# Performance work log

Measured on AMD Instinct MI355X. Metric: run time of the kernel, lower is better.

## Reference

```python
import jax, jax.numpy as jnp
import numpy as np

MODEL_SIZE = 1024
NUM_LAYERS = 8
HEADS = 16
MAX_LENGTH = 4096


def make_alibi_mask(heads, max_len):
    # grid[q,k] = k - q
    grid = (np.arange(max_len)[None, :] - np.arange(max_len)[:, None]).astype(np.float32)
    grid = np.broadcast_to(grid[None, :, :], (heads, max_len, max_len)).copy()
    head_mults = np.power(2.0, -np.linspace(0.0, 8.0, num=heads + 1)[1:]).astype(np.float32)
    grid *= head_mults[:, None, None]
    causal = np.tril(np.ones((max_len, max_len), dtype=np.float32))[None]
    grid = np.where(causal == 0, np.float32(-90000000.0), grid)
    return jnp.asarray(grid)


def layer_norm(x, gamma, beta, eps=1e-3):
    # keras LayerNormalization default epsilon=1e-3
    mu = jnp.mean(x, axis=-1, keepdims=True)
    var = jnp.var(x, axis=-1, keepdims=True)
    return (x - mu) * jax.lax.rsqrt(var + eps) * gamma + beta


def setup_inputs() -> dict:
    key = jax.random.key(0)
    ks = jax.random.split(key, 1 + NUM_LAYERS)
    B, S, D = 2, 2048, MODEL_SIZE
    x = jax.random.normal(ks[0], (B, S, D), dtype=jnp.float32)

    def dense(k, din, dout):
        k1, k2 = jax.random.split(k)
        lim = (6.0 / (din + dout)) ** 0.5
        W = jax.random.uniform(k1, (din, dout), jnp.float32, -lim, lim)
        b = jnp.zeros((dout,), jnp.float32)
        return W, b

    params = []
    for i in range(NUM_LAYERS):
        lk = jax.random.split(ks[1 + i], 5)
        wq, bq = dense(lk[0], D, D)
        wkv, bkv = dense(lk[1], D, 2 * D)
        wo, bo = dense(lk[2], D, D)
        w1, b1 = dense(lk[3], D, 4 * D)
        w2, b2 = dense(lk[4], 4 * D, D)
        ln_att = (jnp.ones((D,), jnp.float32), jnp.zeros((D,), jnp.float32))
        ln_ffn = (jnp.ones((D,), jnp.float32), jnp.zeros((D,), jnp.float32))
        params.append((wq, bq, wkv, bkv, wo, bo, w1, b1, w2, b2,
                       ln_att[0], ln_att[1], ln_ffn[0], ln_ffn[1]))
    final_ln = (jnp.ones((D,), jnp.float32), jnp.zeros((D,), jnp.float32))
    # flatten params into dict
    out = {"target_sequence": x, "final_gamma": final_ln[0], "final_beta": final_ln[1]}
    names = ["wq", "bq", "wkv", "bkv", "wo", "bo", "w1", "b1", "w2", "b2",
             "att_gamma", "att_beta", "ffn_gamma", "ffn_beta"]
    for j, n in enumerate(names):
        out[n] = jnp.stack([params[i][j] for i in range(NUM_LAYERS)])
    return out


def attention(x, wq, bq, wkv, bkv, wo, bo, mask):
    B, S, D = x.shape
    H = HEADS
    hd = D // H
    q = (x @ wq + bq).reshape(B, S, H, hd)
    kv = x @ wkv + bkv
    k, v = jnp.split(kv, 2, axis=-1)
    k = k.reshape(B, S, H, hd)
    v = v.reshape(B, S, H, hd)
    score = jnp.einsum("bqhd,bkhd->bhqk", q, k) * (1.0 / np.sqrt(hd))
    score = score + mask[None]
    attn = jax.nn.softmax(score, axis=-1)
    heads = jnp.einsum("bhqk,bkhd->bqhd", attn, v).reshape(B, S, D)
    return heads @ wo + bo


def reference(target_sequence, wq, bq, wkv, bkv, wo, bo, w1, b1, w2, b2,
              att_gamma, att_beta, ffn_gamma, ffn_beta, final_gamma, final_beta):
    S = target_sequence.shape[1]
    mask = make_alibi_mask(HEADS, MAX_LENGTH)[:, :S, :S]
    x = target_sequence
    for i in range(NUM_LAYERS):
        h = layer_norm(x, att_gamma[i], att_beta[i])
        x = x + attention(h, wq[i], bq[i], wkv[i], bkv[i], wo[i], bo[i], mask)
        h = layer_norm(x, ffn_gamma[i], ffn_beta[i])
        h = jax.nn.softplus(h @ w1[i] + b1[i]) @ w2[i] + b2[i]
        x = x + h
    return layer_norm(x, final_gamma, final_beta)
```

## Files before the change

### kernel.cpp

```cpp
#include <hip/hip_runtime.h>
#include <math.h>

#define DM 1024
#define SEQ 2048
#define BATCH 2
#define NHEAD 16
#define HDIM 64
#define NLAYER 8
#define FFDIM 4096
#define MROWS (BATCH*SEQ)
#define QSTR 3072

typedef __attribute__((ext_vector_type(8))) unsigned short short8;
typedef __attribute__((ext_vector_type(8))) __bf16 bf16x8;
typedef __attribute__((ext_vector_type(4))) float f32x4;

__device__ __forceinline__ float softplus_f(float x){
    const float t = __expf(-fabsf(x));
    return fmaxf(x, 0.0f) + __logf(1.0f + t);
}

__device__ __forceinline__ unsigned short f2bf(float f){
    unsigned u = __builtin_bit_cast(unsigned, f);
    u += 0x7fffu + ((u >> 16) & 1u);
    return (unsigned short)(u >> 16);
}

__device__ __forceinline__ void gload_lds16(const void* g, void* l){
    __builtin_amdgcn_global_load_lds(
        (const __attribute__((address_space(1))) unsigned int*)g,
        (__attribute__((address_space(3))) unsigned int*)l, 16, 0, 0);
}

__global__ __launch_bounds__(256) void tcast_kernel(
    const float* __restrict__ src, unsigned short* __restrict__ dst, int K, int N)
{
    __shared__ float tile[32][33];
    const int bn = blockIdx.x * 32, bk = blockIdx.y * 32;
    const int tx = threadIdx.x & 31, ty = threadIdx.x >> 5;
    #pragma unroll
    for (int i = 0; i < 32; i += 8)
        tile[ty + i][tx] = src[(size_t)(bk + ty + i) * N + bn + tx];
    __syncthreads();
    #pragma unroll
    for (int i = 0; i < 32; i += 8)
        dst[(size_t)(bn + ty + i) * K + bk + tx] = f2bf(tile[tx][ty + i]);
}

__global__ __launch_bounds__(256) void bias_concat_kernel(
    const float* __restrict__ bq, const float* __restrict__ bkv, float* __restrict__ dst)
{
    const int i = blockIdx.x * 256 + threadIdx.x;
    const int l = i / QSTR, c = i % QSTR;
    dst[i] = (c < DM) ? bq[l * DM + c] : bkv[l * 2 * DM + (c - DM)];
}

__global__ __launch_bounds__(256) void vtrans_kernel(
    const unsigned short* __restrict__ qkv, unsigned short* __restrict__ vt)
{
    __shared__ unsigned short tile[64][72];
    const int b  = blockIdx.z;
    const int c0 = blockIdx.x * 64;
    const int s0 = blockIdx.y * 64;
    const int r  = threadIdx.x >> 2;
    const int cq = (threadIdx.x & 3) * 16;
    {
        const unsigned short* src = qkv + (size_t)(b*SEQ + s0 + r) * QSTR + 2*DM + c0 + cq;
        *(uint4*)&tile[r][cq]     = *(const uint4*)(src);
        *(uint4*)&tile[r][cq + 8] = *(const uint4*)(src + 8);
    }
    __syncthreads();
    unsigned short tmp[16];
    #pragma unroll
    for (int j = 0; j < 16; j++) tmp[j] = tile[cq + j][r];
    unsigned short* dst = vt + (size_t)(b*DM + c0 + r) * SEQ + s0 + cq;
    *(uint4*)(dst)     = *(const uint4*)&tmp[0];
    *(uint4*)(dst + 8) = *(const uint4*)&tmp[8];
}

template<bool OUT_BF16>
__global__ __launch_bounds__(256) void ln_kernel(
    const float* __restrict__ x, const float* __restrict__ gamma,
    const float* __restrict__ beta, void* __restrict__ outv)
{
    const int row = blockIdx.x;
    const int t = threadIdx.x;
    const float4 v = ((const float4*)(x + (size_t)row * DM))[t];
    float s  = v.x + v.y + v.z + v.w;
    float s2 = v.x*v.x + v.y*v.y + v.z*v.z + v.w*v.w;
    #pragma unroll
    for (int off = 32; off > 0; off >>= 1){
        s  += __shfl_down(s,  off);
        s2 += __shfl_down(s2, off);
    }
    __shared__ float red[8];
    const int wid = t >> 6;
    if ((t & 63) == 0){ red[wid] = s; red[4 + wid] = s2; }
    __syncthreads();
    if (t == 0){
        red[0] = red[0] + red[1] + red[2] + red[3];
        red[4] = red[4] + red[5] + red[6] + red[7];
    }
    __syncthreads();
    const float mean = red[0] * (1.0f / DM);
    const float var  = red[4] * (1.0f / DM) - mean * mean;
    const float rstd = rsqrtf(var + 1e-3f);
    const float4 g  = ((const float4*)gamma)[t];
    const float4 bt = ((const float4*)beta)[t];
    float ox = (v.x - mean) * rstd * g.x + bt.x;
    float oy = (v.y - mean) * rstd * g.y + bt.y;
    float oz = (v.z - mean) * rstd * g.z + bt.z;
    float ow = (v.w - mean) * rstd * g.w + bt.w;
    if (OUT_BF16){
        ushort4 o = make_ushort4(f2bf(ox), f2bf(oy), f2bf(oz), f2bf(ow));
        *(ushort4*)((unsigned short*)outv + (size_t)row * DM + t*4) = o;
    } else {
        ((float4*)((float*)outv + (size_t)row * DM))[t] = make_float4(ox, oy, oz, ow);
    }
}

template<bool SOFTPLUS, bool RESIDUAL, bool OUT_BF16>
__global__ __launch_bounds__(256) void gemm_bf16_kernel(
    const unsigned short* __restrict__ A, const unsigned short* __restrict__ Bt,
    const float* __restrict__ bias, const float* __restrict__ resid,
    void* __restrict__ Cv, int N, int K)
{
    __shared__ __align__(16) unsigned short As[2][128 * 32];
    __shared__ __align__(16) unsigned short Bs[2][128 * 32];
    const int t = threadIdx.x;
    const int lane = t & 63, w = t >> 6;
    const int bm = blockIdx.y * 128, bn = blockIdx.x * 128;

    const int srow = lane >> 2;
    const int scol = (lane & 3) * 8;
    const unsigned short* a_g0 = A  + (size_t)(bm + w*32 + srow) * K + scol;
    const unsigned short* a_g1 = a_g0 + (size_t)16 * K;
    const unsigned short* b_g0 = Bt + (size_t)(bn + w*32 + srow) * K + scol;
    const unsigned short* b_g1 = b_g0 + (size_t)16 * K;
    const int a_off0 = (w*32     ) * 32;
    const int a_off1 = (w*32 + 16) * 32;

    const int wr = (w >> 1) * 64;
    const int wc = (w & 1) * 64;
    const int fm = lane & 15;
    const int fq = (lane >> 4) * 8;

    f32x4 acc[4][4] = {};

#define STAGE(buf, k0)                                     \
    do {                                                   \
        gload_lds16(a_g0 + (k0), &As[buf][a_off0]);        \
        gload_lds16(a_g1 + (k0), &As[buf][a_off1]);        \
        gload_lds16(b_g0 + (k0), &Bs[buf][a_off0]);        \
        gload_lds16(b_g1 + (k0), &Bs[buf][a_off1]);        \
    } while (0)

#define COMPUTE(buf)                                                        \
    do {                                                                    \
        bf16x8 af[4], bfr[4];                                               \
        _Pragma("unroll")                                                   \
        for (int mi = 0; mi < 4; mi++)                                      \
            af[mi] = __builtin_bit_cast(bf16x8,                             \
                *(const short8*)&As[buf][(wr + mi*16 + fm) * 32 + fq]);     \
        _Pragma("unroll")                                                   \
        for (int ni = 0; ni < 4; ni++)                                      \
            bfr[ni] = __builtin_bit_cast(bf16x8,                            \
                *(const short8*)&Bs[buf][(wc + ni*16 + fm) * 32 + fq]);     \
        _Pragma("unroll")                                                   \
        for (int mi = 0; mi < 4; mi++)                                      \
            _Pragma("unroll")                                               \
            for (int ni = 0; ni < 4; ni++)                                  \
                acc[mi][ni] = __builtin_amdgcn_mfma_f32_16x16x32_bf16(      \
                    af[mi], bfr[ni], acc[mi][ni], 0, 0, 0);                 \
    } while (0)

    STAGE(0, 0);
    __syncthreads();
    for (int k0 = 0; k0 < K; k0 += 64){
        STAGE(1, k0 + 32);
        COMPUTE(0);
        __syncthreads();
        if (k0 + 64 < K) STAGE(0, k0 + 64);
        COMPUTE(1);
        __syncthreads();
    }
#undef STAGE
#undef COMPUTE

    const int crow = (lane >> 4) * 4;
    const int ccol = lane & 15;
    #pragma unroll
    for (int mi = 0; mi < 4; mi++){
        #pragma unroll
        for (int r = 0; r < 4; r++){
            const size_t row = (size_t)bm + wr + mi*16 + crow + r;
            #pragma unroll
            for (int ni = 0; ni < 4; ni++){
                const int col = bn + wc + ni*16 + ccol;
                float v = acc[mi][ni][r] + bias[col];
                if (SOFTPLUS) v = softplus_f(v);
                if (RESIDUAL) v += resid[row * N + col];
                if (OUT_BF16) ((unsigned short*)Cv)[row * N + col] = f2bf(v);
                else          ((float*)Cv)[row * N + col] = v;
            }
        }
    }
}

__global__ __launch_bounds__(256, 4) void attn_kernel(
    const unsigned short* __restrict__ qkv,
    const unsigned short* __restrict__ vt,
    unsigned short* __restrict__ outg)
{
    __shared__ __align__(16) unsigned short Qs[64][72];
    __shared__ __align__(16) unsigned short Ks[64][72];
    __shared__ __align__(16) unsigned short Vt[64][72];
    __shared__ __align__(16) unsigned short Ps[64][72];

    const int L   = blockIdx.x + 32 * (blockIdx.y + 16 * blockIdx.z);
    const int rep = L >> 8, jj = L & 255;
    const int mm  = jj >> 4, h = jj & 15;
    const int b   = rep >> 1;
    const int qt  = (rep & 1) ? (31 - mm) : mm;

    const int t = threadIdx.x;
    const int lane = t & 63, w = t >> 6;
    const int g = lane >> 4, s = lane & 15;

    const size_t qrow0 = (size_t)(b * SEQ + qt * 64);
    const int srow = t >> 2, slc = t & 3;

    {
        const unsigned short* src = qkv + (qrow0 + srow) * QSTR + h*HDIM + slc*16;
        *(uint4*)&Qs[srow][slc*16]     = *(const uint4*)(src);
        *(uint4*)&Qs[srow][slc*16 + 8] = *(const uint4*)(src + 8);
    }
    __syncthreads();
    bf16x8 qf0 = __builtin_bit_cast(bf16x8, *(const short8*)&Qs[w*16 + s][g*8]);
    bf16x8 qf1 = __builtin_bit_cast(bf16x8, *(const short8*)&Qs[w*16 + s][32 + g*8]);

    const float LOG2E  = 1.4426950408889634f;
    const float qscale = 0.125f * LOG2E;
    const float slope  = exp2f(-0.5f * (float)(h + 1)) * LOG2E;
    const int qi = qt*64 + w*16 + s;
    float m_i = -1e30f, l_i = 0.0f;
    f32x4 accO[4] = {};

    const unsigned short* vbase = vt + (size_t)(b*DM + h*HDIM + srow) * SEQ;

    for (int kt = 0; kt <= qt; kt++){
        __syncthreads();
        {
            const unsigned short* src =
                qkv + (size_t)(b*SEQ + kt*64 + srow) * QSTR + DM + h*HDIM + slc*16;
            *(uint4*)&Ks[srow][slc*16]     = *(const uint4*)(src);
            *(uint4*)&Ks[srow][slc*16 + 8] = *(const uint4*)(src + 8);
        }
        {
            const unsigned short* src = vbase + kt*64 + slc*16;
            *(uint4*)&Vt[srow][slc*16]     = *(const uint4*)(src);
            *(uint4*)&Vt[srow][slc*16 + 8] = *(const uint4*)(src + 8);
        }
        __syncthreads();

        f32x4 sacc[4] = {};
        #pragma unroll
        for (int mi = 0; mi < 4; mi++){
            bf16x8 kf0 = __builtin_bit_cast(bf16x8, *(const short8*)&Ks[mi*16 + s][g*8]);
            bf16x8 kf1 = __builtin_bit_cast(bf16x8, *(const short8*)&Ks[mi*16 + s][32 + g*8]);
            sacc[mi] = __builtin_amdgcn_mfma_f32_16x16x32_bf16(kf0, qf0, sacc[mi], 0, 0, 0);
            sacc[mi] = __builtin_amdgcn_mfma_f32_16x16x32_bf16(kf1, qf1, sacc[mi], 0, 0, 0);
        }

        float sc[16];
        const float bb = slope * (float)(kt*64 - qi);
        #pragma unroll
        for (int mi = 0; mi < 4; mi++)
            #pragma unroll
            for (int r = 0; r < 4; r++)
                sc[mi*4 + r] = fmaf(sacc[mi][r], qscale,
                                    fmaf(slope, (float)(mi*16 + g*4 + r), bb));
        if (kt == qt){
            #pragma unroll
            for (int mi = 0; mi < 4; mi++)
                #pragma unroll
                for (int r = 0; r < 4; r++)
                    if (mi*16 + g*4 + r > w*16 + s) sc[mi*4 + r] = -1e30f;
        }
        float mloc = sc[0];
        #pragma unroll
        for (int e = 1; e < 16; e++) mloc = fmaxf(mloc, sc[e]);
        mloc = fmaxf(mloc, __shfl_xor(mloc, 16));
        mloc = fmaxf(mloc, __shfl_xor(mloc, 32));

        float nm;
        if (__all(mloc - m_i <= 8.0f)){
            nm = m_i;
        } else {
            nm = fmaxf(m_i, mloc);
            const float alpha = exp2f(m_i - nm);
            m_i = nm;
            float av[4];
            #pragma unroll
            for (int r = 0; r < 4; r++) av[r] = __shfl(alpha, g*4 + r);
            #pragma unroll
            for (int ni = 0; ni < 4; ni++)
                #pragma unroll
                for (int r = 0; r < 4; r++) accO[ni][r] *= av[r];
            l_i *= alpha;
        }

        float rsum = 0.0f;
        #pragma unroll
        for (int mi = 0; mi < 4; mi++){
            const float p0 = exp2f(sc[mi*4+0] - nm);
            const float p1 = exp2f(sc[mi*4+1] - nm);
            const float p2 = exp2f(sc[mi*4+2] - nm);
            const float p3 = exp2f(sc[mi*4+3] - nm);
            rsum += (p0 + p1) + (p2 + p3);
            *(ushort4*)&Ps[w*16 + s][mi*16 + g*4] =
                make_ushort4(f2bf(p0), f2bf(p1), f2bf(p2), f2bf(p3));
        }
        rsum += __shfl_xor(rsum, 16);
        rsum += __shfl_xor(rsum, 32);
        l_i += rsum;

        bf16x8 pf0 = __builtin_bit_cast(bf16x8, *(const short8*)&Ps[w*16 + s][g*8]);
        bf16x8 pf1 = __builtin_bit_cast(bf16x8, *(const short8*)&Ps[w*16 + s][32 + g*8]);
        #pragma unroll
        for (int ni = 0; ni < 4; ni++){
            bf16x8 vf0 = __builtin_bit_cast(bf16x8, *(const short8*)&Vt[ni*16 + s][g*8]);
            bf16x8 vf1 = __builtin_bit_cast(bf16x8, *(const short8*)&Vt[ni*16 + s][32 + g*8]);
            accO[ni] = __builtin_amdgcn_mfma_f32_16x16x32_bf16(pf0, vf0, accO[ni], 0, 0, 0);
            accO[ni] = __builtin_amdgcn_mfma_f32_16x16x32_bf16(pf1, vf1, accO[ni], 0, 0, 0);
        }
    }

    float lv[4];
    #pragma unroll
    for (int r = 0; r < 4; r++) lv[r] = 1.0f / __shfl(l_i, g*4 + r);
    #pragma unroll
    for (int ni = 0; ni < 4; ni++)
        #pragma unroll
        for (int r = 0; r < 4; r++)
            outg[(qrow0 + w*16 + g*4 + r) * DM + h*HDIM + ni*16 + s] =
                f2bf(accO[ni][r] * lv[r]);
}

extern "C" void kernel_launch(void* const* d_in, const int* in_sizes, int n_in,
                              void* d_out, int out_size, void* d_ws, size_t ws_size,
                              hipStream_t stream)
{
    (void)in_sizes; (void)n_in; (void)out_size; (void)ws_size;

    const float* x_in = (const float*)d_in[0];
    const float* fg   = (const float*)d_in[1];
    const float* fb   = (const float*)d_in[2];
    const float* wq   = (const float*)d_in[3];
    const float* bq   = (const float*)d_in[4];
    const float* wkv  = (const float*)d_in[5];
    const float* bkv  = (const float*)d_in[6];
    const float* wo   = (const float*)d_in[7];
    const float* bo   = (const float*)d_in[8];
    const float* w1   = (const float*)d_in[9];
    const float* b1   = (const float*)d_in[10];
    const float* w2   = (const float*)d_in[11];
    const float* b2   = (const float*)d_in[12];
    const float* attg = (const float*)d_in[13];
    const float* attb = (const float*)d_in[14];
    const float* ffng = (const float*)d_in[15];
    const float* ffnb = (const float*)d_in[16];

    float* x = (float*)d_out;

    char* wp = (char*)d_ws;
    unsigned short* qkvbuf = (unsigned short*)wp; wp += (size_t)MROWS*QSTR*2;
    unsigned short* h1buf  = (unsigned short*)wp; wp += (size_t)MROWS*FFDIM*2;
    unsigned short* hbuf   = (unsigned short*)wp; wp += (size_t)MROWS*DM*2;
    unsigned short* attbuf = (unsigned short*)wp; wp += (size_t)MROWS*DM*2;
    unsigned short* wt_qkv = (unsigned short*)wp; wp += (size_t)QSTR*DM*2;
    unsigned short* wt_o   = (unsigned short*)wp; wp += (size_t)DM*DM*2;
    unsigned short* wt_1   = (unsigned short*)wp; wp += (size_t)FFDIM*DM*2;
    unsigned short* wt_2   = (unsigned short*)wp; wp += (size_t)DM*FFDIM*2;
    float*          qkv_b  = (float*)wp;          wp += (size_t)NLAYER*QSTR*4;

    unsigned short* vtbuf = h1buf;

    hipMemcpyAsync(x, x_in, (size_t)MROWS*DM*sizeof(float),
                   hipMemcpyDeviceToDevice, stream);
    bias_concat_kernel<<<NLAYER*QSTR/256, 256, 0, stream>>>(bq, bkv, qkv_b);

    const dim3 blk(256);
    const dim3 g_qkv(QSTR/128,  MROWS/128);
    const dim3 g_sq (DM/128,    MROWS/128);
    const dim3 g_ff (FFDIM/128, MROWS/128);
    const dim3 g_at (SEQ/64, NHEAD, BATCH);
    const dim3 g_vt (DM/64, SEQ/64, BATCH);

    for (int i = 0; i < NLAYER; i++){
        const float* wq_i  = wq  + (size_t)i*DM*DM;
        const float* wkv_i = wkv + (size_t)i*DM*2*DM;
        const float* wo_i  = wo  + (size_t)i*DM*DM;
        const float* bo_i  = bo  + (size_t)i*DM;
        const float* w1_i  = w1  + (size_t)i*DM*FFDIM;
        const float* b1_i  = b1  + (size_t)i*FFDIM;
        const float* w2_i  = w2  + (size_t)i*FFDIM*DM;
        const float* b2_i  = b2  + (size_t)i*DM;

        tcast_kernel<<<dim3(DM/32,    DM/32),    blk, 0, stream>>>(wq_i,  wt_qkv,         DM,    DM);
        tcast_kernel<<<dim3(2*DM/32,  DM/32),    blk, 0, stream>>>(wkv_i, wt_qkv + DM*DM, DM,    2*DM);
        tcast_kernel<<<dim3(DM/32,    DM/32),    blk, 0, stream>>>(wo_i,  wt_o,           DM,    DM);
        tcast_kernel<<<dim3(FFDIM/32, DM/32),    blk, 0, stream>>>(w1_i,  wt_1,           DM,    FFDIM);
        tcast_kernel<<<dim3(DM/32,    FFDIM/32), blk, 0, stream>>>(w2_i,  wt_2,           FFDIM, DM);

        ln_kernel<true><<<MROWS, blk, 0, stream>>>(x, attg + (size_t)i*DM, attb + (size_t)i*DM, hbuf);
        gemm_bf16_kernel<false,false,true><<<g_qkv, blk, 0, stream>>>(
            hbuf, wt_qkv, qkv_b + (size_t)i*QSTR, nullptr, qkvbuf, QSTR, DM);
        vtrans_kernel<<<g_vt, blk, 0, stream>>>(qkvbuf, vtbuf);
        attn_kernel<<<g_at, blk, 0, stream>>>(qkvbuf, vtbuf, attbuf);
        gemm_bf16_kernel<false,true,false><<<g_sq, blk, 0, stream>>>(
            attbuf, wt_o, bo_i, x, x, DM, DM);
        ln_kernel<true><<<MROWS, blk, 0, stream>>>(x, ffng + (size_t)i*DM, ffnb + (size_t)i*DM, hbuf);
        gemm_bf16_kernel<true,false,true><<<g_ff, blk, 0, stream>>>(
            hbuf, wt_1, b1_i, nullptr, h1buf, FFDIM, DM);
        gemm_bf16_kernel<false,true,false><<<g_sq, blk, 0, stream>>>(
            h1buf, wt_2, b2_i, x, x, DM, FFDIM);
    }
    ln_kernel<false><<<MROWS, blk, 0, stream>>>(x, fg, fb, x);
}
```

Measured before the change: 2.803 ms.

## Restructure bf16 GEMM with BK=64 swizzled LDS, register-prefetch pipeline and block remap

The GEMM K-tile grows from 32 to 64 and the LDS layout gets an XOR swizzle to avoid bank conflicts on fragment reads. The main loop now loads all fragments into registers, then immediately reissues the next global-to-LDS stage into the same buffer so the loads overlap the MFMAs. It uses explicit vmcnt/lgkmcnt waits in place of full syncthreads. Block indices are remapped across groups of 8 for better L2 locality, and launch bounds request 2 blocks per CU. This doubles LDS use (64KB) and raises register pressure.

```diff
diff --git a/kernel.cpp b/kernel.cpp
--- a/kernel.cpp
+++ b/kernel.cpp
@@ -120,72 +120,93 @@
 }
 
 template<bool SOFTPLUS, bool RESIDUAL, bool OUT_BF16>
-__global__ __launch_bounds__(256) void gemm_bf16_kernel(
+__global__ __launch_bounds__(256, 2) void gemm_bf16_kernel(
     const unsigned short* __restrict__ A, const unsigned short* __restrict__ Bt,
     const float* __restrict__ bias, const float* __restrict__ resid,
     void* __restrict__ Cv, int N, int K)
 {
-    __shared__ __align__(16) unsigned short As[2][128 * 32];
-    __shared__ __align__(16) unsigned short Bs[2][128 * 32];
+    __shared__ __align__(16) unsigned short As[2][128 * 64];
+    __shared__ __align__(16) unsigned short Bs[2][128 * 64];
     const int t = threadIdx.x;
     const int lane = t & 63, w = t >> 6;
-    const int bm = blockIdx.y * 128, bn = blockIdx.x * 128;
-
-    const int srow = lane >> 2;
-    const int scol = (lane & 3) * 8;
-    const unsigned short* a_g0 = A  + (size_t)(bm + w*32 + srow) * K + scol;
-    const unsigned short* a_g1 = a_g0 + (size_t)16 * K;
-    const unsigned short* b_g0 = Bt + (size_t)(bn + w*32 + srow) * K + scol;
-    const unsigned short* b_g1 = b_g0 + (size_t)16 * K;
-    const int a_off0 = (w*32     ) * 32;
-    const int a_off1 = (w*32 + 16) * 32;
+
+    const int gx = gridDim.x;
+    const int nwg = gx * gridDim.y;
+    int bid = blockIdx.x + gx * blockIdx.y;
+    bid = (bid & 7) * (nwg >> 3) + (bid >> 3);
+    const int bm = (bid / gx) * 128, bn = (bid % gx) * 128;
+
+    const int srow  = w*8 + (lane >> 3);
+    const int sslot = (lane & 7) ^ (lane >> 3);
+    const unsigned short* a_g = A  + (size_t)(bm + srow) * K + sslot * 8;
+    const unsigned short* b_g = Bt + (size_t)(bn + srow) * K + sslot * 8;
 
     const int wr = (w >> 1) * 64;
     const int wc = (w & 1) * 64;
     const int fm = lane & 15;
-    const int fq = (lane >> 4) * 8;
+    const int q  = lane >> 4;
+    const int f7 = fm & 7;
 
     f32x4 acc[4][4] = {};
-
-#define STAGE(buf, k0)                                     \
-    do {                                                   \
-        gload_lds16(a_g0 + (k0), &As[buf][a_off0]);        \
-        gload_lds16(a_g1 + (k0), &As[buf][a_off1]);        \
-        gload_lds16(b_g0 + (k0), &Bs[buf][a_off0]);        \
-        gload_lds16(b_g1 + (k0), &Bs[buf][a_off1]);        \
+    const int ntile = K >> 6;
+
+#define STAGE(buf, k0)                                                      \
+    do {                                                                    \
+        _Pragma("unroll")                                                   \
+        for (int j = 0; j < 4; j++){                                        \
+            gload_lds16(a_g + (size_t)(j*32)*K + (k0), &As[buf][(j*32 + w*8)*64]); \
+            gload_lds16(b_g + (size_t)(j*32)*K + (k0), &Bs[buf][(j*32 + w*8)*64]); \
+        }                                                                   \
     } while (0)
 
-#define COMPUTE(buf)                                                        \
-    do {                                                                    \
-        bf16x8 af[4], bfr[4];                                               \
+#define LOADFRAGS(buf)                                                      \
+    _Pragma("unroll")                                                       \
+    for (int kk2 = 0; kk2 < 2; kk2++){                                      \
         _Pragma("unroll")                                                   \
         for (int mi = 0; mi < 4; mi++)                                      \
-            af[mi] = __builtin_bit_cast(bf16x8,                             \
-                *(const short8*)&As[buf][(wr + mi*16 + fm) * 32 + fq]);     \
+            af[kk2][mi] = __builtin_bit_cast(bf16x8, *(const short8*)       \
+                &As[buf][(wr + mi*16 + fm)*64 + (((kk2*4 + q) ^ f7) << 3)]);\
         _Pragma("unroll")                                                   \
         for (int ni = 0; ni < 4; ni++)                                      \
-            bfr[ni] = __builtin_bit_cast(bf16x8,                            \
-                *(const short8*)&Bs[buf][(wc + ni*16 + fm) * 32 + fq]);     \
+            bfm[kk2][ni] = __builtin_bit_cast(bf16x8, *(const short8*)      \
+                &Bs[buf][(wc + ni*16 + fm)*64 + (((kk2*4 + q) ^ f7) << 3)]);\
+    }
+
+#define MFMAS()                                                             \
+    _Pragma("unroll")                                                       \
+    for (int kk2 = 0; kk2 < 2; kk2++)                                       \
         _Pragma("unroll")                                                   \
         for (int mi = 0; mi < 4; mi++)                                      \
             _Pragma("unroll")                                               \
             for (int ni = 0; ni < 4; ni++)                                  \
                 acc[mi][ni] = __builtin_amdgcn_mfma_f32_16x16x32_bf16(      \
-                    af[mi], bfr[ni], acc[mi][ni], 0, 0, 0);                 \
-    } while (0)
+                    af[kk2][mi], bfm[kk2][ni], acc[mi][ni], 0, 0, 0);
 
     STAGE(0, 0);
-    __syncthreads();
-    for (int k0 = 0; k0 < K; k0 += 64){
-        STAGE(1, k0 + 32);
-        COMPUTE(0);
-        __syncthreads();
-        if (k0 + 64 < K) STAGE(0, k0 + 64);
-        COMPUTE(1);
-        __syncthreads();
+    STAGE(1, 64);
+
+    int cur = 0;
+    for (int td = 0; td < ntile - 1; ++td){
+        asm volatile("s_waitcnt vmcnt(8)" ::: "memory");
+        __builtin_amdgcn_s_barrier();
+        bf16x8 af[2][4], bfm[2][4];
+        LOADFRAGS(cur);
+        asm volatile("s_waitcnt lgkmcnt(0)" ::: "memory");
+        __builtin_amdgcn_s_barrier();
+        if (td + 2 < ntile) STAGE(cur, (td + 2) * 64);
+        MFMAS();
+        cur ^= 1;
+    }
+    {
+        asm volatile("s_waitcnt vmcnt(0)" ::: "memory");
+        __builtin_amdgcn_s_barrier();
+        bf16x8 af[2][4], bfm[2][4];
+        LOADFRAGS(cur);
+        MFMAS();
     }
 #undef STAGE
-#undef COMPUTE
+#undef LOADFRAGS
+#undef MFMAS
 
     const int crow = (lane >> 4) * 4;
     const int ccol = lane & 15;
```

Measured after the change: 2.268 ms. -19.1%, faster.
